# Performance work log

Measured on AMD Instinct MI355X. Metric: run time of the kernel, lower is better.

The kernel has to match this reference:

```python
import jax, jax.numpy as jnp
import numpy as np

HID = 128
N_NODES = 50000
N_EDGES = 640000
N_GRAPHS = 64
N_LAYERS = 3
LN_EPS = 1e-5


def _ln(h, g, b):
    mu = jnp.mean(h, axis=-1, keepdims=True)
    v = jnp.mean(jnp.square(h - mu), axis=-1, keepdims=True)
    return (h - mu) * jax.lax.rsqrt(v + LN_EPS) * g + b


def _mlp2(h, W1, b1, g, be, W2, b2):
    # Linear -> ReLU -> LayerNorm -> (Dropout=identity in eval) -> Linear
    h = _ln(jax.nn.relu(h @ W1.T + b1), g, be)
    return h @ W2.T + b2


def _forward(x, edge_index, batch, axis_W1, axis_b1, axis_g, axis_be, axis_W2, axis_b2, org_W1, org_b1, org_g, org_be, org_W2, org_b2, nin_W, nin_b, conv_W1, conv_b1, conv_g, conv_be, conv_W2, conv_b2, eps, ln_g, ln_b, gate_W1, gate_b1, gate_g, gate_be, gate_W2, gate_b2, head_W1, head_b1, head_g, head_be, head_W2, head_b2):
    axis = x[:, 9:12]
    origin = x[:, 12:15]
    others = jnp.concatenate([x[:, :9], x[:, 15:19]], axis=1)  # [N, 13]
    axis_z = _mlp2(axis, axis_W1, axis_b1, axis_g, axis_be, axis_W2, axis_b2)
    org_z = _mlp2(origin, org_W1, org_b1, org_g, org_be, org_W2, org_b2)
    h = jnp.concatenate([others, axis_z, org_z], axis=1) @ nin_W.T + nin_b  # [N, HID]
    src, dst = edge_index[0], edge_index[1]
    n = x.shape[0]
    for l in range(N_LAYERS):
        res = h
        # GIN: sum-aggregate source features into targets (gather + scatter-add)
        agg = jax.ops.segment_sum(h[src], dst, num_segments=n)
        m = (1.0 + eps[l]) * h + agg
        m = _mlp2(m, conv_W1[l], conv_b1[l], conv_g[l], conv_be[l], conv_W2[l], conv_b2[l])
        h = _ln(jax.nn.relu(m), ln_g[l], ln_b[l]) + res
    # AttentionalAggregation: segment softmax over per-graph node gates
    gate = _mlp2(h, gate_W1, gate_b1, gate_g, gate_be, gate_W2, gate_b2)  # [N, 1]
    gmax = jax.ops.segment_max(gate, batch, num_segments=N_GRAPHS)
    e = jnp.exp(gate - gmax[batch])
    denom = jax.ops.segment_sum(e, batch, num_segments=N_GRAPHS)
    attn = e / denom[batch]
    g = jax.ops.segment_sum(attn * h, batch, num_segments=N_GRAPHS)  # [B, HID]
    logit = _mlp2(g, head_W1, head_b1, head_g, head_be, head_W2, head_b2)[:, 0]
    return logit


def setup_inputs() -> dict:
    key = jax.random.key(0)
    ks = iter(jax.random.split(key, 64))
    nk = lambda: next(ks)
    lin = lambda o, i: jax.random.normal(nk(), (o, i), jnp.float32) / np.float32(np.sqrt(i))
    lin3 = lambda L, o, i: jnp.stack([lin(o, i) for _ in range(L)])
    z = lambda *s: jnp.zeros(s, jnp.float32)
    o = lambda *s: jnp.ones(s, jnp.float32)
    inp = {}
    inp['x'] = jax.random.normal(nk(), (N_NODES, 19), jnp.float32)
    inp['edge_index'] = jax.random.randint(nk(), (2, N_EDGES), 0, N_NODES)
    inp['batch'] = jnp.sort(jax.random.randint(nk(), (N_NODES,), 0, N_GRAPHS))
    for p in ('axis', 'org'):
        inp[p + '_W1'] = lin(16, 3); inp[p + '_b1'] = z(16)
        inp[p + '_g'] = o(16); inp[p + '_be'] = z(16)
        inp[p + '_W2'] = lin(16, 16); inp[p + '_b2'] = z(16)
    inp['nin_W'] = lin(HID, 45); inp['nin_b'] = z(HID)
    inp['conv_W1'] = lin3(N_LAYERS, HID, HID); inp['conv_b1'] = z(N_LAYERS, HID)
    inp['conv_g'] = o(N_LAYERS, HID); inp['conv_be'] = z(N_LAYERS, HID)
    inp['conv_W2'] = lin3(N_LAYERS, HID, HID); inp['conv_b2'] = z(N_LAYERS, HID)
    inp['eps'] = z(N_LAYERS)
    inp['ln_g'] = o(N_LAYERS, HID); inp['ln_b'] = z(N_LAYERS, HID)
    for p in ('gate', 'head'):
        inp[p + '_W1'] = lin(HID // 2, HID); inp[p + '_b1'] = z(HID // 2)
        inp[p + '_g'] = o(HID // 2); inp[p + '_be'] = z(HID // 2)
        inp[p + '_W2'] = lin(1, HID // 2); inp[p + '_b2'] = z(1)
    return inp


def reference(x, edge_index, batch, axis_W1, axis_b1, axis_g, axis_be, axis_W2, axis_b2, org_W1, org_b1, org_g, org_be, org_W2, org_b2, nin_W, nin_b, conv_W1, conv_b1, conv_g, conv_be, conv_W2, conv_b2, eps, ln_g, ln_b, gate_W1, gate_b1, gate_g, gate_be, gate_W2, gate_b2, head_W1, head_b1, head_g, head_be, head_W2, head_b2):
    return _forward(x, edge_index, batch, axis_W1, axis_b1, axis_g, axis_be, axis_W2, axis_b2, org_W1, org_b1, org_g, org_be, org_W2, org_b2, nin_W, nin_b, conv_W1, conv_b1, conv_g, conv_be, conv_W2, conv_b2, eps, ln_g, ln_b, gate_W1, gate_b1, gate_g, gate_be, gate_W2, gate_b2, head_W1, head_b1, head_g, head_be, head_W2, head_b2)
```

## Files before the change

kernel.cpp:

```cpp
#include <hip/hip_runtime.h>

#define N_NODESC 50000
#define N_EDGESC 640000
#define N_GRAPHSC 64
#define HIDC 128
#define LN_EPSF 1e-5f
#define POOL_SPLIT 16
#define SCAN_NB 49
#define EGRID ((N_EDGESC + 255) / 256)
#define NGRID_GB ((N_NODESC + 255) / 256)
#define NGRID64 ((N_NODESC + 63) / 64)
#define PREP_ELEMS (8192 + 49152 + 49152)
#define WPREP_NB ((PREP_ELEMS + 255) / 256)
#define CSTR 32

typedef short bf16x8 __attribute__((ext_vector_type(8)));
typedef float f32x4 __attribute__((ext_vector_type(4)));

static __device__ __forceinline__ unsigned ord_enc(float f) {
  unsigned u = __float_as_uint(f);
  return (u & 0x80000000u) ? ~u : (u | 0x80000000u);
}
static __device__ __forceinline__ float ord_dec(unsigned u) {
  return __uint_as_float((u & 0x80000000u) ? (u ^ 0x80000000u) : ~u);
}
static __device__ __forceinline__ unsigned short f2bf(float x) {
  unsigned u = __float_as_uint(x);
  u += 0x7fffu + ((u >> 16) & 1u);
  return (unsigned short)(u >> 16);
}
static __device__ __forceinline__ float bf2f(unsigned short b) {
  return __uint_as_float(((unsigned)b) << 16);
}

static __device__ __forceinline__ void mlp16(float in0, float in1, float in2,
    const float* __restrict__ W1, const float* __restrict__ b1,
    const float* __restrict__ g, const float* __restrict__ be,
    const float* __restrict__ W2, const float* __restrict__ b2,
    float* __restrict__ out) {
  float h[16];
  float s1 = 0.f, s2 = 0.f;
#pragma unroll
  for (int j = 0; j < 16; ++j) {
    float v = b1[j] + W1[j*3+0]*in0 + W1[j*3+1]*in1 + W1[j*3+2]*in2;
    v = fmaxf(v, 0.f);
    h[j] = v; s1 += v; s2 += v*v;
  }
  float mu = s1 * (1.f/16.f);
  float var = fmaxf(s2 * (1.f/16.f) - mu*mu, 0.f);
  float rs = rsqrtf(var + LN_EPSF);
  float z[16];
#pragma unroll
  for (int j = 0; j < 16; ++j) z[j] = (h[j]-mu)*rs*g[j] + be[j];
#pragma unroll
  for (int j = 0; j < 16; ++j) {
    float v = b2[j];
#pragma unroll
    for (int k = 0; k < 16; ++k) v += W2[j*16+k]*z[k];
    out[j] = v;
  }
}

__global__ __launch_bounds__(256) void hist_gbound_kernel(const int* __restrict__ ei,
    int* __restrict__ deg_p, const int* __restrict__ batch, int* __restrict__ gstart,
    const float* __restrict__ ninW, unsigned short* __restrict__ ninWb,
    const float* __restrict__ cW1, unsigned short* __restrict__ cW1b,
    const float* __restrict__ cW2, unsigned short* __restrict__ cW2b) {
  const int b = blockIdx.x;
  if (b < EGRID) {
    int e = b * 256 + threadIdx.x;
    if (e < N_EDGESC) atomicAdd(&deg_p[ei[N_EDGESC + e] * CSTR], 1);
  } else if (b < EGRID + NGRID_GB) {
    int i = (b - EGRID) * 256 + threadIdx.x;
    if (i >= N_NODESC) return;
    int bb = batch[i];
    int prev = (i == 0) ? -1 : batch[i-1];
    for (int g = prev + 1; g <= bb; ++g) gstart[g] = i;
    if (i == N_NODESC - 1) {
      for (int g = bb + 1; g <= N_GRAPHSC; ++g) gstart[g] = N_NODESC;
    }
  } else {
    int i = (b - EGRID - NGRID_GB) * 256 + threadIdx.x;
    if (i < 8192) {
      int f = i >> 6, k = i & 63;
      ninWb[i] = (k < 45) ? f2bf(ninW[f*45 + k]) : (unsigned short)0;
    } else if (i < 8192 + 49152) {
      int j = i - 8192;
      cW1b[j] = f2bf(cW1[j]);
    } else if (i < PREP_ELEMS) {
      int j = i - 8192 - 49152;
      cW2b[j] = f2bf(cW2[j]);
    }
  }
}

__global__ __launch_bounds__(1024) void scan1_kernel(const int* __restrict__ deg_p,
                                                     int* __restrict__ incl,
                                                     int* __restrict__ bsum) {
  const int b = blockIdx.x, t = threadIdx.x;
  const int i = b * 1024 + t;
  const int lane = t & 63, w = t >> 6;
  int v = (i < N_NODESC) ? deg_p[i * CSTR] : 0;
#pragma unroll
  for (int off = 1; off < 64; off <<= 1) {
    int n = __shfl_up(v, off);
    if (lane >= off) v += n;
  }
  __shared__ int wsum[16];
  if (lane == 63) wsum[w] = v;
  __syncthreads();
  if (t == 0) {
    int run = 0;
#pragma unroll
    for (int k = 0; k < 16; ++k) { int x = wsum[k]; wsum[k] = run; run += x; }
  }
  __syncthreads();
  v += wsum[w];
  if (i < N_NODESC) incl[i] = v;
  if (t == 1023) bsum[b] = v;
}

__global__ __launch_bounds__(1024) void scan23_kernel(const int* __restrict__ deg_p,
                                                      const int* __restrict__ bsum,
                                                      int* __restrict__ rowptr,
                                                      int* __restrict__ cursor_p) {
  __shared__ int ex[SCAN_NB + 1];
  const int b = blockIdx.x, t = threadIdx.x;
  if (t < 64) {
    int v = (t < SCAN_NB) ? bsum[t] : 0;
    const int orig = v;
#pragma unroll
    for (int off = 1; off < 64; off <<= 1) {
      int n = __shfl_up(v, off);
      if (t >= off) v += n;
    }
    if (t < SCAN_NB) ex[t] = v - orig;
    if (t == SCAN_NB - 1) ex[SCAN_NB] = v;
  }
  __syncthreads();
  const int i = b * 1024 + t;
  if (i < N_NODESC) {
    int excl = rowptr[i] - deg_p[i * CSTR] + ex[b];
    rowptr[i] = excl;
    cursor_p[i * CSTR] = excl;
  }
  if (b == 0 && t == 0) rowptr[N_NODESC] = ex[SCAN_NB];
}

__global__ __launch_bounds__(256, 4) void scatter_enc_kernel(
    const int* __restrict__ ei, int* __restrict__ cursor_p, int* __restrict__ esrc,
    const float* __restrict__ x,
    const float* __restrict__ aW1, const float* __restrict__ ab1,
    const float* __restrict__ ag,  const float* __restrict__ abe,
    const float* __restrict__ aW2, const float* __restrict__ ab2,
    const float* __restrict__ oW1, const float* __restrict__ ob1,
    const float* __restrict__ og,  const float* __restrict__ obe,
    const float* __restrict__ oW2, const float* __restrict__ ob2,
    const unsigned short* __restrict__ ninWb, const float* __restrict__ ninb,
    unsigned short* __restrict__ Hb) {
  __shared__ unsigned short Ab[64*136];
  const int t = threadIdx.x;

  if (blockIdx.x < EGRID) {
    int e = blockIdx.x * 256 + t;
    if (e < N_EDGESC) {
      int d = ei[N_EDGESC + e];
      int slot = atomicAdd(&cursor_p[d * CSTR], 1);
      esrc[slot] = ei[e];
    }
    return;
  }

  const int nb = (blockIdx.x - EGRID) * 64;

  if (t < 192) {
    const int n = t & 63;
    const int gn = nb + n;
    const int grp = t >> 6;
    if (gn < N_NODESC) {
      const float* xr = x + gn * 19;
      if (grp == 0) {
        float z[16];
        mlp16(xr[9], xr[10], xr[11], aW1, ab1, ag, abe, aW2, ab2, z);
#pragma unroll
        for (int k = 0; k < 16; ++k) Ab[n*136 + 13 + k] = f2bf(z[k]);
      } else if (grp == 1) {
        float z[16];
        mlp16(xr[12], xr[13], xr[14], oW1, ob1, og, obe, oW2, ob2, z);
#pragma unroll
        for (int k = 0; k < 16; ++k) Ab[n*136 + 29 + k] = f2bf(z[k]);
      } else {
#pragma unroll
        for (int k = 0; k < 9; ++k) Ab[n*136 + k] = f2bf(xr[k]);
#pragma unroll
        for (int k = 0; k < 4; ++k) Ab[n*136 + 9 + k] = f2bf(xr[15 + k]);
#pragma unroll
        for (int k = 45; k < 64; ++k) Ab[n*136 + k] = 0;
      }
    } else {
      if (grp == 0) {
#pragma unroll
        for (int k = 0; k < 16; ++k) Ab[n*136 + 13 + k] = 0;
      } else if (grp == 1) {
#pragma unroll
        for (int k = 0; k < 16; ++k) Ab[n*136 + 29 + k] = 0;
      } else {
#pragma unroll
        for (int k = 0; k < 13; ++k) Ab[n*136 + k] = 0;
#pragma unroll
        for (int k = 45; k < 64; ++k) Ab[n*136 + k] = 0;
      }
    }
  }
  __syncthreads();

  const int lane = t & 63, wv = t >> 6;
  const int quad = lane >> 4, l16 = lane & 15;
  const int arow = (wv*16 + l16)*136 + quad*8;
  f32x4 acc[8];
#pragma unroll
  for (int ft = 0; ft < 8; ++ft) acc[ft] = (f32x4){0.f,0.f,0.f,0.f};
#pragma unroll
  for (int ks = 0; ks < 2; ++ks) {
    bf16x8 a = *(const bf16x8*)(const void*)&Ab[arow + ks*32];
#pragma unroll
    for (int ft = 0; ft < 8; ++ft) {
      bf16x8 bfr = *(const bf16x8*)&ninWb[(ft*16 + l16)*64 + quad*8 + ks*32];
      acc[ft] = __builtin_amdgcn_mfma_f32_16x16x32_bf16(a, bfr, acc[ft], 0, 0, 0);
    }
  }
  float bb[8];
#pragma unroll
  for (int ft = 0; ft < 8; ++ft) bb[ft] = ninb[ft*16 + l16];
  __syncthreads();
#pragma unroll
  for (int r = 0; r < 4; ++r) {
    int nloc = wv*16 + quad*4 + r;
#pragma unroll
    for (int ft = 0; ft < 8; ++ft)
      Ab[nloc*136 + ft*16 + l16] = f2bf(acc[ft][r] + bb[ft]);
  }
  __syncthreads();
#pragma unroll
  for (int i = 0; i < 4; ++i) {
    int chunk = t + i*256;
    int n = chunk >> 4, c8 = chunk & 15;
    int gn = nb + n;
    if (gn < N_NODESC)
      *(bf16x8*)&Hb[gn*HIDC + c8*8] = *(const bf16x8*)&Ab[n*136 + c8*8];
  }
}

__global__ __launch_bounds__(128) void agg_kernel(const unsigned short* __restrict__ Hb,
    const int* __restrict__ rowptr, const int* __restrict__ esrc,
    const float* __restrict__ epsp, unsigned short* __restrict__ Mb) {
  const int t = threadIdx.x;
  const int c8 = t & 15;
  const int v  = t >> 4;
  const int node = blockIdx.x * 8 + v;
  if (node >= N_NODESC) return;
  const float e1 = 1.0f + epsp[0];
  bf16x8 h = *(const bf16x8*)&Hb[node*HIDC + c8*8];
  float acc[8];
#pragma unroll
  for (int k = 0; k < 8; ++k) acc[k] = 0.f;
  int s = rowptr[node];
  const int e = rowptr[node+1];
  for (; s + 8 <= e; s += 8) {
    int i0 = esrc[s],   i1 = esrc[s+1], i2 = esrc[s+2], i3 = esrc[s+3];
    int i4 = esrc[s+4], i5 = esrc[s+5], i6 = esrc[s+6], i7 = esrc[s+7];
    bf16x8 x0 = *(const bf16x8*)&Hb[i0*HIDC + c8*8];
    bf16x8 x1 = *(const bf16x8*)&Hb[i1*HIDC + c8*8];
    bf16x8 x2 = *(const bf16x8*)&Hb[i2*HIDC + c8*8];
    bf16x8 x3 = *(const bf16x8*)&Hb[i3*HIDC + c8*8];
    bf16x8 x4 = *(const bf16x8*)&Hb[i4*HIDC + c8*8];
    bf16x8 x5 = *(const bf16x8*)&Hb[i5*HIDC + c8*8];
    bf16x8 x6 = *(const bf16x8*)&Hb[i6*HIDC + c8*8];
    bf16x8 x7 = *(const bf16x8*)&Hb[i7*HIDC + c8*8];
#pragma unroll
    for (int k = 0; k < 8; ++k)
      acc[k] += ((bf2f((unsigned short)x0[k]) + bf2f((unsigned short)x1[k]))
               + (bf2f((unsigned short)x2[k]) + bf2f((unsigned short)x3[k])))
              + ((bf2f((unsigned short)x4[k]) + bf2f((unsigned short)x5[k]))
               + (bf2f((unsigned short)x6[k]) + bf2f((unsigned short)x7[k])));
  }
  for (; s + 4 <= e; s += 4) {
    int i0 = esrc[s], i1 = esrc[s+1], i2 = esrc[s+2], i3 = esrc[s+3];
    bf16x8 x0 = *(const bf16x8*)&Hb[i0*HIDC + c8*8];
    bf16x8 x1 = *(const bf16x8*)&Hb[i1*HIDC + c8*8];
    bf16x8 x2 = *(const bf16x8*)&Hb[i2*HIDC + c8*8];
    bf16x8 x3 = *(const bf16x8*)&Hb[i3*HIDC + c8*8];
#pragma unroll
    for (int k = 0; k < 8; ++k)
      acc[k] += (bf2f((unsigned short)x0[k]) + bf2f((unsigned short)x1[k]))
              + (bf2f((unsigned short)x2[k]) + bf2f((unsigned short)x3[k]));
  }
  for (; s < e; ++s) {
    bf16x8 x0 = *(const bf16x8*)&Hb[esrc[s]*HIDC + c8*8];
#pragma unroll
    for (int k = 0; k < 8; ++k) acc[k] += bf2f((unsigned short)x0[k]);
  }
  bf16x8 m8;
#pragma unroll
  for (int k = 0; k < 8; ++k)
    m8[k] = (short)f2bf(e1*bf2f((unsigned short)h[k]) + acc[k]);
  *(bf16x8*)&Mb[node*HIDC + c8*8] = m8;
}

template<bool GATE>
__global__ __launch_bounds__(256, 3) void gemmpair_kernel(
    const unsigned short* __restrict__ Mb,
    const unsigned short* __restrict__ Hin,
    const unsigned short* __restrict__ W1b, const float* __restrict__ b1,
    const float* __restrict__ g1, const float* __restrict__ be1,
    const unsigned short* __restrict__ W2b, const float* __restrict__ b2,
    const float* __restrict__ lng, const float* __restrict__ lnb,
    unsigned short* __restrict__ Hout,
    const float* __restrict__ gW1, const float* __restrict__ gb1,
    const float* __restrict__ glng, const float* __restrict__ glnb,
    const float* __restrict__ gW2, const float* __restrict__ gb2,
    const int* __restrict__ batch, float* __restrict__ gateb,
    unsigned* __restrict__ gmaxu) {
  __shared__ unsigned short Ab[64*136];
  __shared__ unsigned short Wl[128*136];
  __shared__ unsigned sgm[N_GRAPHSC];
  const int t = threadIdx.x;
  const int nb = blockIdx.x * 64;
  if (GATE && t < N_GRAPHSC) sgm[t] = 0u;

#pragma unroll
  for (int i = 0; i < 4; ++i) {
    int chunk = t + i*256;
    int n = chunk >> 4, c8 = chunk & 15;
    int gn = nb + n;
    bf16x8 v = {0,0,0,0,0,0,0,0};
    if (gn < N_NODESC) v = *(const bf16x8*)&Mb[gn*HIDC + c8*8];
    *(bf16x8*)&Ab[n*136 + c8*8] = v;
  }
#pragma unroll
  for (int i = 0; i < 8; ++i) {
    int q = t + i*256;
    int f = q >> 4, c8 = q & 15;
    *(bf16x8*)&Wl[f*136 + c8*8] = *(const bf16x8*)&W1b[f*HIDC + c8*8];
  }
  __syncthreads();

  const int lane = t & 63, wv = t >> 6;
  const int quad = lane >> 4, l16 = lane & 15;
  const int arow = (wv*16 + l16)*136 + quad*8;

  f32x4 acc[8];
#pragma unroll
  for (int ft = 0; ft < 8; ++ft) acc[ft] = (f32x4){0.f,0.f,0.f,0.f};
#pragma unroll
  for (int ks = 0; ks < 4; ++ks) {
    bf16x8 a = *(const bf16x8*)(const void*)&Ab[arow + ks*32];
#pragma unroll
    for (int ft = 0; ft < 8; ++ft) {
      bf16x8 b = *(const bf16x8*)(const void*)&Wl[(ft*16 + l16)*136 + quad*8 + ks*32];
      acc[ft] = __builtin_amdgcn_mfma_f32_16x16x32_bf16(a, b, acc[ft], 0, 0, 0);
    }
  }

  {
    float bb[8], gg[8], bee[8];
#pragma unroll
    for (int ft = 0; ft < 8; ++ft) {
      int f = ft*16 + l16;
      bb[ft] = b1[f]; gg[ft] = g1[f]; bee[ft] = be1[f];
    }
    float s1[4] = {0,0,0,0}, s2[4] = {0,0,0,0};
#pragma unroll
    for (int ft = 0; ft < 8; ++ft)
#pragma unroll
      for (int r = 0; r < 4; ++r) {
        float v = fmaxf(acc[ft][r] + bb[ft], 0.f);
        acc[ft][r] = v; s1[r] += v; s2[r] += v*v;
      }
#pragma unroll
    for (int m = 1; m < 16; m <<= 1)
#pragma unroll
      for (int r = 0; r < 4; ++r) {
        s1[r] += __shfl_xor(s1[r], m);
        s2[r] += __shfl_xor(s2[r], m);
      }
    float mu[4], rs[4];
#pragma unroll
    for (int r = 0; r < 4; ++r) {
      mu[r] = s1[r] * (1.f/128.f);
      float var = fmaxf(s2[r] * (1.f/128.f) - mu[r]*mu[r], 0.f);
      rs[r] = rsqrtf(var + LN_EPSF);
    }
    __syncthreads();
#pragma unroll
    for (int r = 0; r < 4; ++r) {
      int nloc = wv*16 + quad*4 + r;
#pragma unroll
      for (int ft = 0; ft < 8; ++ft) {
        float o = (acc[ft][r] - mu[r])*rs[r]*gg[ft] + bee[ft];
        Ab[nloc*136 + ft*16 + l16] = f2bf(o);
      }
    }
  }
#pragma unroll
  for (int i = 0; i < 8; ++i) {
    int q = t + i*256;
    int f = q >> 4, c8 = q & 15;
    *(bf16x8*)&Wl[f*136 + c8*8] = *(const bf16x8*)&W2b[f*HIDC + c8*8];
  }
  __syncthreads();

#pragma unroll
  for (int ft = 0; ft < 8; ++ft) acc[ft] = (f32x4){0.f,0.f,0.f,0.f};
#pragma unroll
  for (int ks = 0; ks < 4; ++ks) {
    bf16x8 a = *(const bf16x8*)(const void*)&Ab[arow + ks*32];
#pragma unroll
    for (int ft = 0; ft < 8; ++ft) {
      bf16x8 b = *(const bf16x8*)(const void*)&Wl[(ft*16 + l16)*136 + quad*8 + ks*32];
      acc[ft] = __builtin_amdgcn_mfma_f32_16x16x32_bf16(a, b, acc[ft], 0, 0, 0);
    }
  }

  {
    float bb[8], gg[8], bee[8];
#pragma unroll
    for (int ft = 0; ft < 8; ++ft) {
      int f = ft*16 + l16;
      bb[ft] = b2[f]; gg[ft] = lng[f]; bee[ft] = lnb[f];
    }
    float s1[4] = {0,0,0,0}, s2[4] = {0,0,0,0};
#pragma unroll
    for (int ft = 0; ft < 8; ++ft)
#pragma unroll
      for (int r = 0; r < 4; ++r) {
        float v = fmaxf(acc[ft][r] + bb[ft], 0.f);
        acc[ft][r] = v; s1[r] += v; s2[r] += v*v;
      }
#pragma unroll
    for (int m = 1; m < 16; m <<= 1)
#pragma unroll
      for (int r = 0; r < 4; ++r) {
        s1[r] += __shfl_xor(s1[r], m);
        s2[r] += __shfl_xor(s2[r], m);
      }
    float mu[4], rs[4];
#pragma unroll
    for (int r = 0; r < 4; ++r) {
      mu[r] = s1[r] * (1.f/128.f);
      float var = fmaxf(s2[r] * (1.f/128.f) - mu[r]*mu[r], 0.f);
      rs[r] = rsqrtf(var + LN_EPSF);
    }
    __syncthreads();
#pragma unroll
    for (int r = 0; r < 4; ++r) {
      int nloc = wv*16 + quad*4 + r;
#pragma unroll
      for (int ft = 0; ft < 8; ++ft) {
        float o = (acc[ft][r] - mu[r])*rs[r]*gg[ft] + bee[ft];
        Ab[nloc*136 + ft*16 + l16] = f2bf(o);
      }
    }
  }
  __syncthreads();
#pragma unroll
  for (int i = 0; i < 4; ++i) {
    int chunk = t + i*256;
    int n = chunk >> 4, cc = chunk & 15;
    int gn = nb + n;
    bf16x8 o8 = {0,0,0,0,0,0,0,0};
    if (gn < N_NODESC) {
      bf16x8 vv = *(const bf16x8*)&Ab[n*136 + cc*8];
      bf16x8 rr = *(const bf16x8*)&Hin[gn*HIDC + cc*8];
#pragma unroll
      for (int k = 0; k < 8; ++k)
        o8[k] = (short)f2bf(bf2f((unsigned short)vv[k]) + bf2f((unsigned short)rr[k]));
      *(bf16x8*)&Hout[gn*HIDC + cc*8] = o8;
    }
    if (GATE) *(bf16x8*)&Ab[n*136 + cc*8] = o8;
  }

  if (GATE) {
#pragma unroll
    for (int i = 0; i < 8; ++i) {
      int q = t + i*256;
      int f = q >> 5, c4 = q & 31;
      float4 v = *(const float4*)&gW1[f*HIDC + c4*4];
      ushort4 hh;
      hh.x = f2bf(v.x); hh.y = f2bf(v.y); hh.z = f2bf(v.z); hh.w = f2bf(v.w);
      *(ushort4*)&Wl[f*136 + c4*4] = hh;
    }
    __syncthreads();

    f32x4 gacc[4];
#pragma unroll
    for (int ft = 0; ft < 4; ++ft) gacc[ft] = (f32x4){0.f,0.f,0.f,0.f};
#pragma unroll
    for (int ks = 0; ks < 4; ++ks) {
      bf16x8 a = *(const bf16x8*)(const void*)&Ab[arow + ks*32];
#pragma unroll
      for (int ft = 0; ft < 4; ++ft) {
        bf16x8 b = *(const bf16x8*)(const void*)&Wl[(ft*16 + l16)*136 + quad*8 + ks*32];
        gacc[ft] = __builtin_amdgcn_mfma_f32_16x16x32_bf16(a, b, gacc[ft], 0, 0, 0);
      }
    }

    float bb[4], gg[4], bee[4], w2v[4];
#pragma unroll
    for (int ft = 0; ft < 4; ++ft) {
      int f = ft*16 + l16;
      bb[ft] = gb1[f]; gg[ft] = glng[f]; bee[ft] = glnb[f]; w2v[ft] = gW2[f];
    }
    float s1[4] = {0,0,0,0}, s2[4] = {0,0,0,0};
#pragma unroll
    for (int ft = 0; ft < 4; ++ft)
#pragma unroll
      for (int r = 0; r < 4; ++r) {
        float v = fmaxf(gacc[ft][r] + bb[ft], 0.f);
        gacc[ft][r] = v; s1[r] += v; s2[r] += v*v;
      }
#pragma unroll
    for (int m = 1; m < 16; m <<= 1)
#pragma unroll
      for (int r = 0; r < 4; ++r) {
        s1[r] += __shfl_xor(s1[r], m);
        s2[r] += __shfl_xor(s2[r], m);
      }
    float pd[4];
#pragma unroll
    for (int r = 0; r < 4; ++r) {
      float mu = s1[r] * (1.f/64.f);
      float var = fmaxf(s2[r] * (1.f/64.f) - mu*mu, 0.f);
      float rs = rsqrtf(var + LN_EPSF);
      float p = 0.f;
#pragma unroll
      for (int ft = 0; ft < 4; ++ft)
        p += ((gacc[ft][r] - mu)*rs*gg[ft] + bee[ft]) * w2v[ft];
      pd[r] = p;
    }
#pragma unroll
    for (int m = 1; m < 16; m <<= 1)
#pragma unroll
      for (int r = 0; r < 4; ++r) pd[r] += __shfl_xor(pd[r], m);
    if (l16 == 0) {
      float b2v = gb2[0];
#pragma unroll
      for (int r = 0; r < 4; ++r) {
        int node = nb + wv*16 + quad*4 + r;
        if (node < N_NODESC) {
          float gv = pd[r] + b2v;
          gateb[node] = gv;
          atomicMax(&sgm[batch[node]], ord_enc(gv));
        }
      }
    }
    __syncthreads();
    if (t < N_GRAPHSC && sgm[t] != 0u) atomicMax(&gmaxu[t], sgm[t]);
  }
}

__global__ __launch_bounds__(256) void pool_kernel(const unsigned short* __restrict__ Hb,
    const float* __restrict__ gateb, const int* __restrict__ gstart,
    const unsigned* __restrict__ gmaxu, float* __restrict__ S,
    float* __restrict__ denom) {
  const int g    = blockIdx.x / POOL_SPLIT;
  const int part = blockIdx.x % POOL_SPLIT;
  const int s0 = gstart[g], s1 = gstart[g+1];
  const int cnt = s1 - s0;
  const int chunk = (cnt + POOL_SPLIT - 1) / POOL_SPLIT;
  int lo = s0 + part * chunk;
  int hi = lo + chunk; if (hi > s1) hi = s1;
  const int t = threadIdx.x;
  const int c8 = t & 15;
  const int v  = t >> 4;
  const float gm = ord_dec(gmaxu[g]);
  float acc[8];
#pragma unroll
  for (int k = 0; k < 8; ++k) acc[k] = 0.f;
  float de = 0.f;
  for (int n = lo + v; n < hi; n += 16) {
    float e = expf(gateb[n] - gm);
    bf16x8 hv = *(const bf16x8*)&Hb[n*HIDC + c8*8];
#pragma unroll
    for (int k = 0; k < 8; ++k) acc[k] += e * bf2f((unsigned short)hv[k]);
    if (c8 == 0) de += e;
  }
  __shared__ float sacc[16*128];
  __shared__ float sden[16];
#pragma unroll
  for (int k = 0; k < 8; ++k) sacc[v*128 + c8*8 + k] = acc[k];
  if (c8 == 0) sden[v] = de;
  __syncthreads();
  if (t < 128) {
    float s = 0.f;
#pragma unroll
    for (int vv = 0; vv < 16; ++vv) s += sacc[vv*128 + t];
    atomicAdd(&S[g*HIDC + t], s);
  }
  if (t == 0) {
    float d = 0.f;
#pragma unroll
    for (int vv = 0; vv < 16; ++vv) d += sden[vv];
    atomicAdd(&denom[g], d);
  }
}

__global__ __launch_bounds__(64) void head_kernel(const float* __restrict__ S,
    const float* __restrict__ denom, const float* __restrict__ W1,
    const float* __restrict__ b1, const float* __restrict__ g,
    const float* __restrict__ be, const float* __restrict__ W2,
    const float* __restrict__ b2, float* __restrict__ out) {
  const int gr = blockIdx.x;
  const int j = threadIdx.x;
  const float inv = 1.0f / denom[gr];
  float v = b1[j];
  for (int k = 0; k < HIDC; ++k) v += (S[gr*HIDC + k] * inv) * W1[j*HIDC + k];
  v = fmaxf(v, 0.f);
  float s1 = v, s2 = v*v;
  for (int off = 32; off; off >>= 1) { s1 += __shfl_xor(s1, off); s2 += __shfl_xor(s2, off); }
  float mu = s1 * (1.f/64.f);
  float var = fmaxf(s2 * (1.f/64.f) - mu*mu, 0.f);
  float rs = rsqrtf(var + LN_EPSF);
  float z = (v-mu)*rs*g[j] + be[j];
  float p = z * W2[j];
  for (int off = 32; off; off >>= 1) p += __shfl_xor(p, off);
  if (j == 0) out[gr] = p + b2[0];
}

extern "C" void kernel_launch(void* const* d_in, const int* in_sizes, int n_in,
                              void* d_out, int out_size, void* d_ws, size_t ws_size,
                              hipStream_t stream) {
  (void)in_sizes; (void)n_in; (void)out_size; (void)ws_size;
  const float* x     = (const float*)d_in[0];
  const int*   ei    = (const int*)d_in[1];
  const int*   batch = (const int*)d_in[2];
  const float* aW1 = (const float*)d_in[3];
  const float* ab1 = (const float*)d_in[4];
  const float* ag  = (const float*)d_in[5];
  const float* abe = (const float*)d_in[6];
  const float* aW2 = (const float*)d_in[7];
  const float* ab2 = (const float*)d_in[8];
  const float* oW1 = (const float*)d_in[9];
  const float* ob1 = (const float*)d_in[10];
  const float* og  = (const float*)d_in[11];
  const float* obe = (const float*)d_in[12];
  const float* oW2 = (const float*)d_in[13];
  const float* ob2 = (const float*)d_in[14];
  const float* ninW = (const float*)d_in[15];
  const float* ninb = (const float*)d_in[16];
  const float* cW1 = (const float*)d_in[17];
  const float* cb1 = (const float*)d_in[18];
  const float* cg  = (const float*)d_in[19];
  const float* cbe = (const float*)d_in[20];
  const float* cW2 = (const float*)d_in[21];
  const float* cb2 = (const float*)d_in[22];
  const float* eps = (const float*)d_in[23];
  const float* lng = (const float*)d_in[24];
  const float* lnb = (const float*)d_in[25];
  const float* gW1 = (const float*)d_in[26];
  const float* gb1 = (const float*)d_in[27];
  const float* gg  = (const float*)d_in[28];
  const float* gbe = (const float*)d_in[29];
  const float* gW2 = (const float*)d_in[30];
  const float* gb2 = (const float*)d_in[31];
  const float* hW1 = (const float*)d_in[32];
  const float* hb1 = (const float*)d_in[33];
  const float* hg  = (const float*)d_in[34];
  const float* hbe = (const float*)d_in[35];
  const float* hW2 = (const float*)d_in[36];
  const float* hb2 = (const float*)d_in[37];

  char* ws = (char*)d_ws;
  unsigned short* Ha = (unsigned short*)(ws + 0);
  unsigned short* Hc = (unsigned short*)(ws + 12800000);
  unsigned short* Mb = (unsigned short*)(ws + 25600000);
  int* deg_p    = (int*)(ws + 25600000);
  int* cursor_p = (int*)(ws + 32000000);
  float* gateb = (float*)(ws + 38400000);
  float* S     = (float*)(ws + 38800000);
  float* denom = (float*)(ws + 38832768);
  unsigned* gmaxu = (unsigned*)(ws + 38833024);
  int* rowptr  = (int*)(ws + 38833280);
  int* esrc    = (int*)(ws + 39233284);
  int* bsum    = (int*)(ws + 41793284);
  int* gstart  = (int*)(ws + 41793540);
  unsigned short* ninWb = (unsigned short*)(ws + 41800000);
  unsigned short* cW1b  = (unsigned short*)(ws + 41816384);
  unsigned short* cW2b  = (unsigned short*)(ws + 41914688);

  hipMemsetAsync(deg_p, 0, 6400000, stream);
  hipMemsetAsync(S, 0, 33280, stream);

  hist_gbound_kernel<<<EGRID + NGRID_GB + WPREP_NB, 256, 0, stream>>>(
      ei, deg_p, batch, gstart, ninW, ninWb, cW1, cW1b, cW2, cW2b);
  scan1_kernel<<<SCAN_NB, 1024, 0, stream>>>(deg_p, rowptr, bsum);
  scan23_kernel<<<SCAN_NB, 1024, 0, stream>>>(deg_p, bsum, rowptr, cursor_p);
  scatter_enc_kernel<<<EGRID + NGRID64, 256, 0, stream>>>(
      ei, cursor_p, esrc,
      x, aW1, ab1, ag, abe, aW2, ab2,
      oW1, ob1, og, obe, oW2, ob2,
      ninWb, ninb, Ha);

  unsigned short* cur = Ha;
  unsigned short* nxt = Hc;
  for (int l = 0; l < 3; ++l) {
    agg_kernel<<<(N_NODESC + 7) / 8, 128, 0, stream>>>(cur, rowptr, esrc, eps + l, Mb);
    if (l < 2) {
      gemmpair_kernel<false><<<NGRID64, 256, 0, stream>>>(
          Mb, cur,
          cW1b + l*HIDC*HIDC, cb1 + l*HIDC, cg + l*HIDC, cbe + l*HIDC,
          cW2b + l*HIDC*HIDC, cb2 + l*HIDC, lng + l*HIDC, lnb + l*HIDC,
          nxt,
          gW1, gb1, gg, gbe, gW2, gb2, batch, gateb, gmaxu);
    } else {
      gemmpair_kernel<true><<<NGRID64, 256, 0, stream>>>(
          Mb, cur,
          cW1b + l*HIDC*HIDC, cb1 + l*HIDC, cg + l*HIDC, cbe + l*HIDC,
          cW2b + l*HIDC*HIDC, cb2 + l*HIDC, lng + l*HIDC, lnb + l*HIDC,
          nxt,
          gW1, gb1, gg, gbe, gW2, gb2, batch, gateb, gmaxu);
    }
    unsigned short* tmp = cur; cur = nxt; nxt = tmp;
  }

  pool_kernel<<<N_GRAPHSC * POOL_SPLIT, 256, 0, stream>>>(Hc, gateb, gstart, gmaxu, S, denom);
  head_kernel<<<N_GRAPHSC, 64, 0, stream>>>(S, denom, hW1, hb1, hg, hbe, hW2, hb2,
                                            (float*)d_out);
}
```

Baseline: 363.1 us.

## Build CSR via two-level bucket sort instead of global atomic histogram

Replaces the per-node global atomic degree histogram, the padded cursor arrays and the two-stage scan with a two-level binning scheme. Edges are first counted and scattered into coarse 512-node buckets using shared-memory atomics, and each bucket then builds its own rowptr and esrc with LDS histograms and scans. This removes the 6.4MB memset and the heavily contended global atomics on padded counters. In exchange it adds an extra pass over the edges through an intermediate pairs buffer and launches more kernels.

Result: faster. 331.8 us (-8.6%).

```diff
diff --git a/kernel.cpp b/kernel.cpp
--- a/kernel.cpp
+++ b/kernel.cpp
@@ -6,13 +6,14 @@
 #define HIDC 128
 #define LN_EPSF 1e-5f
 #define POOL_SPLIT 16
-#define SCAN_NB 49
-#define EGRID ((N_EDGESC + 255) / 256)
 #define NGRID_GB ((N_NODESC + 255) / 256)
 #define NGRID64 ((N_NODESC + 63) / 64)
 #define PREP_ELEMS (8192 + 49152 + 49152)
 #define WPREP_NB ((PREP_ELEMS + 255) / 256)
-#define CSTR 32
+#define B1C 200
+#define BCHUNK 3200
+#define NBUK 98
+#define WBUK 512
 
 typedef short bf16x8 __attribute__((ext_vector_type(8)));
 typedef float f32x4 __attribute__((ext_vector_type(4)));
@@ -61,26 +62,34 @@
   }
 }
 
-__global__ __launch_bounds__(256) void hist_gbound_kernel(const int* __restrict__ ei,
-    int* __restrict__ deg_p, const int* __restrict__ batch, int* __restrict__ gstart,
+__global__ __launch_bounds__(256) void bin_count_kernel(const int* __restrict__ ei,
+    int* __restrict__ counts, const int* __restrict__ batch, int* __restrict__ gstart,
     const float* __restrict__ ninW, unsigned short* __restrict__ ninWb,
     const float* __restrict__ cW1, unsigned short* __restrict__ cW1b,
     const float* __restrict__ cW2, unsigned short* __restrict__ cW2b) {
   const int b = blockIdx.x;
-  if (b < EGRID) {
-    int e = b * 256 + threadIdx.x;
-    if (e < N_EDGESC) atomicAdd(&deg_p[ei[N_EDGESC + e] * CSTR], 1);
-  } else if (b < EGRID + NGRID_GB) {
-    int i = (b - EGRID) * 256 + threadIdx.x;
+  if (b < B1C) {
+    __shared__ int cnt[NBUK];
+    for (int i = threadIdx.x; i < NBUK; i += 256) cnt[i] = 0;
+    __syncthreads();
+    const int e0 = b * BCHUNK;
+    const int e1 = e0 + BCHUNK;
+    for (int e = e0 + threadIdx.x; e < e1; e += 256)
+      atomicAdd(&cnt[ei[N_EDGESC + e] >> 9], 1);
+    __syncthreads();
+    for (int i = threadIdx.x; i < NBUK; i += 256)
+      counts[i * B1C + b] = cnt[i];
+  } else if (b < B1C + NGRID_GB) {
+    int i = (b - B1C) * 256 + threadIdx.x;
     if (i >= N_NODESC) return;
-    int bb = batch[i];
+    int bb_ = batch[i];
     int prev = (i == 0) ? -1 : batch[i-1];
-    for (int g = prev + 1; g <= bb; ++g) gstart[g] = i;
+    for (int g = prev + 1; g <= bb_; ++g) gstart[g] = i;
     if (i == N_NODESC - 1) {
-      for (int g = bb + 1; g <= N_GRAPHSC; ++g) gstart[g] = N_NODESC;
+      for (int g = bb_ + 1; g <= N_GRAPHSC; ++g) gstart[g] = N_NODESC;
     }
   } else {
-    int i = (b - EGRID - NGRID_GB) * 256 + threadIdx.x;
+    int i = (b - B1C - NGRID_GB) * 256 + threadIdx.x;
     if (i < 8192) {
       int f = i >> 6, k = i & 63;
       ninWb[i] = (k < 45) ? f2bf(ninW[f*45 + k]) : (unsigned short)0;
@@ -94,61 +103,54 @@
   }
 }
 
-__global__ __launch_bounds__(1024) void scan1_kernel(const int* __restrict__ deg_p,
-                                                     int* __restrict__ incl,
-                                                     int* __restrict__ bsum) {
-  const int b = blockIdx.x, t = threadIdx.x;
-  const int i = b * 1024 + t;
+__global__ __launch_bounds__(256) void bin_scanA_kernel(const int* __restrict__ counts,
+                                                        int* __restrict__ offl,
+                                                        int* __restrict__ btot) {
+  const int buk = blockIdx.x, t = threadIdx.x;
   const int lane = t & 63, w = t >> 6;
-  int v = (i < N_NODESC) ? deg_p[i * CSTR] : 0;
+  int v = (t < B1C) ? counts[buk * B1C + t] : 0;
+  const int orig = v;
 #pragma unroll
   for (int off = 1; off < 64; off <<= 1) {
     int n = __shfl_up(v, off);
     if (lane >= off) v += n;
   }
-  __shared__ int wsum[16];
+  __shared__ int wsum[4];
   if (lane == 63) wsum[w] = v;
   __syncthreads();
   if (t == 0) {
     int run = 0;
 #pragma unroll
-    for (int k = 0; k < 16; ++k) { int x = wsum[k]; wsum[k] = run; run += x; }
-  }
-  __syncthreads();
-  v += wsum[w];
-  if (i < N_NODESC) incl[i] = v;
-  if (t == 1023) bsum[b] = v;
-}
-
-__global__ __launch_bounds__(1024) void scan23_kernel(const int* __restrict__ deg_p,
-                                                      const int* __restrict__ bsum,
-                                                      int* __restrict__ rowptr,
-                                                      int* __restrict__ cursor_p) {
-  __shared__ int ex[SCAN_NB + 1];
-  const int b = blockIdx.x, t = threadIdx.x;
-  if (t < 64) {
-    int v = (t < SCAN_NB) ? bsum[t] : 0;
-    const int orig = v;
-#pragma unroll
-    for (int off = 1; off < 64; off <<= 1) {
-      int n = __shfl_up(v, off);
-      if (t >= off) v += n;
-    }
-    if (t < SCAN_NB) ex[t] = v - orig;
-    if (t == SCAN_NB - 1) ex[SCAN_NB] = v;
-  }
-  __syncthreads();
-  const int i = b * 1024 + t;
-  if (i < N_NODESC) {
-    int excl = rowptr[i] - deg_p[i * CSTR] + ex[b];
-    rowptr[i] = excl;
-    cursor_p[i * CSTR] = excl;
-  }
-  if (b == 0 && t == 0) rowptr[N_NODESC] = ex[SCAN_NB];
-}
-
-__global__ __launch_bounds__(256, 4) void scatter_enc_kernel(
-    const int* __restrict__ ei, int* __restrict__ cursor_p, int* __restrict__ esrc,
+    for (int k = 0; k < 4; ++k) { int x = wsum[k]; wsum[k] = run; run += x; }
+  }
+  __syncthreads();
+  int incl = v + wsum[w];
+  if (t < B1C) offl[buk * B1C + t] = incl - orig;
+  if (t == 255) btot[buk] = incl;
+}
+
+__global__ __launch_bounds__(128) void bin_scanB_kernel(const int* __restrict__ btot,
+                                                        int* __restrict__ bb) {
+  const int t = threadIdx.x, lane = t & 63, w = t >> 6;
+  int v = (t < NBUK) ? btot[t] : 0;
+  const int orig = v;
+#pragma unroll
+  for (int off = 1; off < 64; off <<= 1) {
+    int n = __shfl_up(v, off);
+    if (lane >= off) v += n;
+  }
+  __shared__ int ws2[2];
+  if (lane == 63) ws2[w] = v;
+  __syncthreads();
+  int add = (w == 1) ? ws2[0] : 0;
+  int excl = v + add - orig;
+  if (t < NBUK) bb[t] = excl;
+  if (t == 0) bb[NBUK] = N_EDGESC;
+}
+
+__global__ __launch_bounds__(256, 4) void bin_write_enc_kernel(
+    const int* __restrict__ ei, const int* __restrict__ offl, const int* __restrict__ bb,
+    int2* __restrict__ pairs,
     const float* __restrict__ x,
     const float* __restrict__ aW1, const float* __restrict__ ab1,
     const float* __restrict__ ag,  const float* __restrict__ abe,
@@ -161,17 +163,22 @@
   __shared__ unsigned short Ab[64*136];
   const int t = threadIdx.x;
 
-  if (blockIdx.x < EGRID) {
-    int e = blockIdx.x * 256 + t;
-    if (e < N_EDGESC) {
-      int d = ei[N_EDGESC + e];
-      int slot = atomicAdd(&cursor_p[d * CSTR], 1);
-      esrc[slot] = ei[e];
+  if (blockIdx.x < B1C) {
+    int* cur = (int*)Ab;
+    const int blk = blockIdx.x;
+    for (int i = t; i < NBUK; i += 256) cur[i] = bb[i] + offl[i * B1C + blk];
+    __syncthreads();
+    const int e0 = blk * BCHUNK;
+    const int e1 = e0 + BCHUNK;
+    for (int e = e0 + t; e < e1; e += 256) {
+      int s = ei[e], d = ei[N_EDGESC + e];
+      int pos = atomicAdd(&cur[d >> 9], 1);
+      pairs[pos] = make_int2(s, d);
     }
     return;
   }
 
-  const int nb = (blockIdx.x - EGRID) * 64;
+  const int nb = (blockIdx.x - B1C) * 64;
 
   if (t < 192) {
     const int n = t & 63;
@@ -229,16 +236,16 @@
       acc[ft] = __builtin_amdgcn_mfma_f32_16x16x32_bf16(a, bfr, acc[ft], 0, 0, 0);
     }
   }
-  float bb[8];
-#pragma unroll
-  for (int ft = 0; ft < 8; ++ft) bb[ft] = ninb[ft*16 + l16];
+  float bbv[8];
+#pragma unroll
+  for (int ft = 0; ft < 8; ++ft) bbv[ft] = ninb[ft*16 + l16];
   __syncthreads();
 #pragma unroll
   for (int r = 0; r < 4; ++r) {
     int nloc = wv*16 + quad*4 + r;
 #pragma unroll
     for (int ft = 0; ft < 8; ++ft)
-      Ab[nloc*136 + ft*16 + l16] = f2bf(acc[ft][r] + bb[ft]);
+      Ab[nloc*136 + ft*16 + l16] = f2bf(acc[ft][r] + bbv[ft]);
   }
   __syncthreads();
 #pragma unroll
@@ -249,6 +256,68 @@
     if (gn < N_NODESC)
       *(bf16x8*)&Hb[gn*HIDC + c8*8] = *(const bf16x8*)&Ab[n*136 + c8*8];
   }
+}
+
+__global__ __launch_bounds__(256) void bucket_build_kernel(const int2* __restrict__ pairs,
+    const int* __restrict__ bb, int* __restrict__ rowptr, int* __restrict__ esrc) {
+  __shared__ int hist[WBUK];
+  __shared__ int wsum[4];
+  __shared__ int totS;
+  const int b = blockIdx.x, t = threadIdx.x;
+  const int lane = t & 63, w = t >> 6;
+  const int node0 = b * WBUK;
+  for (int i = t; i < WBUK; i += 256) hist[i] = 0;
+  __syncthreads();
+  const int base = bb[b], end = bb[b + 1];
+  for (int p = base + t; p < end; p += 256)
+    atomicAdd(&hist[pairs[p].y - node0], 1);
+  __syncthreads();
+  const int v0 = hist[t], v1 = hist[256 + t];
+  int a = v0;
+#pragma unroll
+  for (int off = 1; off < 64; off <<= 1) {
+    int n = __shfl_up(a, off);
+    if (lane >= off) a += n;
+  }
+  if (lane == 63) wsum[w] = a;
+  __syncthreads();
+  if (t == 0) {
+    int run = 0;
+#pragma unroll
+    for (int k = 0; k < 4; ++k) { int x = wsum[k]; wsum[k] = run; run += x; }
+    totS = run;
+  }
+  __syncthreads();
+  const int e0 = a + wsum[w] - v0;
+  const int tot0 = totS;
+  __syncthreads();
+  int c = v1;
+#pragma unroll
+  for (int off = 1; off < 64; off <<= 1) {
+    int n = __shfl_up(c, off);
+    if (lane >= off) c += n;
+  }
+  if (lane == 63) wsum[w] = c;
+  __syncthreads();
+  if (t == 0) {
+    int run = 0;
+#pragma unroll
+    for (int k = 0; k < 4; ++k) { int x = wsum[k]; wsum[k] = run; run += x; }
+  }
+  __syncthreads();
+  const int e1 = tot0 + c + wsum[w] - v1;
+  hist[t] = e0;
+  hist[256 + t] = e1;
+  const int n0 = node0 + t, n1 = node0 + 256 + t;
+  if (n0 < N_NODESC) rowptr[n0] = base + e0;
+  if (n1 < N_NODESC) rowptr[n1] = base + e1;
+  __syncthreads();
+  for (int p = base + t; p < end; p += 256) {
+    int2 pr = pairs[p];
+    int slot = base + atomicAdd(&hist[pr.y - node0], 1);
+    esrc[slot] = pr.x;
+  }
+  if (b == NBUK - 1 && t == 0) rowptr[N_NODESC] = N_EDGESC;
 }
 
 __global__ __launch_bounds__(128) void agg_kernel(const unsigned short* __restrict__ Hb,
@@ -363,18 +432,18 @@
   }
 
   {
-    float bb[8], gg[8], bee[8];
+    float bbv[8], gg[8], bee[8];
 #pragma unroll
     for (int ft = 0; ft < 8; ++ft) {
       int f = ft*16 + l16;
-      bb[ft] = b1[f]; gg[ft] = g1[f]; bee[ft] = be1[f];
+      bbv[ft] = b1[f]; gg[ft] = g1[f]; bee[ft] = be1[f];
     }
     float s1[4] = {0,0,0,0}, s2[4] = {0,0,0,0};
 #pragma unroll
     for (int ft = 0; ft < 8; ++ft)
 #pragma unroll
       for (int r = 0; r < 4; ++r) {
-        float v = fmaxf(acc[ft][r] + bb[ft], 0.f);
+        float v = fmaxf(acc[ft][r] + bbv[ft], 0.f);
         acc[ft][r] = v; s1[r] += v; s2[r] += v*v;
       }
 #pragma unroll
@@ -423,18 +492,18 @@
   }
 
   {
-    float bb[8], gg[8], bee[8];
+    float bbv[8], gg[8], bee[8];
 #pragma unroll
     for (int ft = 0; ft < 8; ++ft) {
       int f = ft*16 + l16;
-      bb[ft] = b2[f]; gg[ft] = lng[f]; bee[ft] = lnb[f];
+      bbv[ft] = b2[f]; gg[ft] = lng[f]; bee[ft] = lnb[f];
     }
     float s1[4] = {0,0,0,0}, s2[4] = {0,0,0,0};
 #pragma unroll
     for (int ft = 0; ft < 8; ++ft)
 #pragma unroll
       for (int r = 0; r < 4; ++r) {
-        float v = fmaxf(acc[ft][r] + bb[ft], 0.f);
+        float v = fmaxf(acc[ft][r] + bbv[ft], 0.f);
         acc[ft][r] = v; s1[r] += v; s2[r] += v*v;
       }
 #pragma unroll
@@ -505,18 +574,18 @@
       }
     }
 
-    float bb[4], gg[4], bee[4], w2v[4];
+    float bbv[4], gg[4], bee[4], w2v[4];
 #pragma unroll
     for (int ft = 0; ft < 4; ++ft) {
       int f = ft*16 + l16;
-      bb[ft] = gb1[f]; gg[ft] = glng[f]; bee[ft] = glnb[f]; w2v[ft] = gW2[f];
+      bbv[ft] = gb1[f]; gg[ft] = glng[f]; bee[ft] = glnb[f]; w2v[ft] = gW2[f];
     }
     float s1[4] = {0,0,0,0}, s2[4] = {0,0,0,0};
 #pragma unroll
     for (int ft = 0; ft < 4; ++ft)
 #pragma unroll
       for (int r = 0; r < 4; ++r) {
-        float v = fmaxf(gacc[ft][r] + bb[ft], 0.f);
+        float v = fmaxf(gacc[ft][r] + bbv[ft], 0.f);
         gacc[ft][r] = v; s1[r] += v; s2[r] += v*v;
       }
 #pragma unroll
@@ -674,32 +743,34 @@
   unsigned short* Ha = (unsigned short*)(ws + 0);
   unsigned short* Hc = (unsigned short*)(ws + 12800000);
   unsigned short* Mb = (unsigned short*)(ws + 25600000);
-  int* deg_p    = (int*)(ws + 25600000);
-  int* cursor_p = (int*)(ws + 32000000);
+  int2* pairs  = (int2*)(ws + 25600000);
+  int* counts  = (int*)(ws + 30720000);
+  int* offl    = (int*)(ws + 30800000);
+  int* btot    = (int*)(ws + 30880000);
+  int* bb      = (int*)(ws + 30881024);
   float* gateb = (float*)(ws + 38400000);
   float* S     = (float*)(ws + 38800000);
   float* denom = (float*)(ws + 38832768);
   unsigned* gmaxu = (unsigned*)(ws + 38833024);
   int* rowptr  = (int*)(ws + 38833280);
   int* esrc    = (int*)(ws + 39233284);
-  int* bsum    = (int*)(ws + 41793284);
   int* gstart  = (int*)(ws + 41793540);
   unsigned short* ninWb = (unsigned short*)(ws + 41800000);
   unsigned short* cW1b  = (unsigned short*)(ws + 41816384);
   unsigned short* cW2b  = (unsigned short*)(ws + 41914688);
 
-  hipMemsetAsync(deg_p, 0, 6400000, stream);
   hipMemsetAsync(S, 0, 33280, stream);
 
-  hist_gbound_kernel<<<EGRID + NGRID_GB + WPREP_NB, 256, 0, stream>>>(
-      ei, deg_p, batch, gstart, ninW, ninWb, cW1, cW1b, cW2, cW2b);
-  scan1_kernel<<<SCAN_NB, 1024, 0, stream>>>(deg_p, rowptr, bsum);
-  scan23_kernel<<<SCAN_NB, 1024, 0, stream>>>(deg_p, bsum, rowptr, cursor_p);
-  scatter_enc_kernel<<<EGRID + NGRID64, 256, 0, stream>>>(
-      ei, cursor_p, esrc,
+  bin_count_kernel<<<B1C + NGRID_GB + WPREP_NB, 256, 0, stream>>>(
+      ei, counts, batch, gstart, ninW, ninWb, cW1, cW1b, cW2, cW2b);
+  bin_scanA_kernel<<<NBUK, 256, 0, stream>>>(counts, offl, btot);
+  bin_scanB_kernel<<<1, 128, 0, stream>>>(btot, bb);
+  bin_write_enc_kernel<<<B1C + NGRID64, 256, 0, stream>>>(
+      ei, offl, bb, pairs,
       x, aW1, ab1, ag, abe, aW2, ab2,
       oW1, ob1, og, obe, oW2, ob2,
       ninWb, ninb, Ha);
+  bucket_build_kernel<<<NBUK, 256, 0, stream>>>(pairs, bb, rowptr, esrc);
 
   unsigned short* cur = Ha;
   unsigned short* nxt = Hc;
```
